# Kernel optimization log

Hardware: AMD Instinct MI355X
Metric: run time of the kernel (lower is better)

The kernel has to match this reference:

```python
import jax, jax.numpy as jnp
import numpy as np

N, E = 50000, 800000
IN_DIM, HID, OUT_DIM = 128, 96, 64
MAX_REC = 5


def setup_inputs() -> dict:
    key = jax.random.key(0)
    ks = jax.random.split(key, 10)
    g = lambda k, shape, scale: (jax.random.normal(k, shape, jnp.float32) * scale)
    return {
        "x": jax.random.normal(ks[0], (N, IN_DIM), jnp.float32),
        "edge_index": jax.random.randint(ks[1], (2, E), 0, N, jnp.int32),
        "w_in": g(ks[2], (IN_DIM, HID), 0.05),
        "b_in": jnp.zeros((HID,), jnp.float32),
        "tau_w1": g(ks[3], (IN_DIM, 16), 0.08),
        "tau_b1": jnp.zeros((16,), jnp.float32),
        "tau_w2": g(ks[4], (16, 1), 0.25),
        "tau_b2": jnp.zeros((1,), jnp.float32),
        "gru_wih": g(ks[5], (3 * HID, HID), 0.05),
        "gru_whh": g(ks[6], (3 * HID, HID), 0.05),
        "gru_bih": jnp.zeros((3 * HID,), jnp.float32),
        "gru_bhh": jnp.zeros((3 * HID,), jnp.float32),
        "w_out": g(ks[7], (HID, OUT_DIM), 0.05),
        "b_out": jnp.zeros((OUT_DIM,), jnp.float32),
    }


def _gru_cell(inp, h, wih, whh, bih, bhh):
    # torch.nn.GRUCell math; wih/whh are [3H, H] stacked (r, z, n)
    gi = inp @ wih.T + bih  # [N, 3H]
    gh = h @ whh.T + bhh    # [N, 3H]
    ir, iz, inn = jnp.split(gi, 3, axis=-1)
    hr, hz, hn = jnp.split(gh, 3, axis=-1)
    r = jax.nn.sigmoid(ir + hr)
    z = jax.nn.sigmoid(iz + hz)
    n = jnp.tanh(inn + r * hn)
    return (1.0 - z) * n + z * h


def reference(x, edge_index, w_in, b_in, tau_w1, tau_b1, tau_w2, tau_b2,
              gru_wih, gru_whh, gru_bih, gru_bhh, w_out, b_out):
    h = jax.nn.relu(x @ w_in + b_in)  # [N, H]
    tau_val = jax.nn.softplus(jax.nn.relu(x @ tau_w1 + tau_b1) @ tau_w2 + tau_b2)[:, 0]
    # .long() truncates toward zero; tau > 0 so trunc == floor via int cast
    steps = jnp.minimum((1.0 / tau_val).astype(jnp.int32), MAX_REC)  # [N]
    row, col = edge_index[0], edge_index[1]
    for _ in range(MAX_REC):
        d1 = jnp.abs(h[row] - h[col])                       # [E, H]
        agg = jax.ops.segment_sum(d1, row, num_segments=N)  # [N, H]
        new_h = _gru_cell(agg, h, gru_wih, gru_whh, gru_bih, gru_bhh)
        h = jnp.where((steps > 0)[:, None], new_h, h)
        steps = steps - 1
    return h @ w_out + b_out
```

## Files before the change

kernel.cpp:

```cpp
#include <hip/hip_runtime.h>
#include <hip/hip_bf16.h>

#define HID 96
#define INDIM 128
#define OUTDIM 64
#define BM 128
#define GP 128

typedef __attribute__((ext_vector_type(8))) _Float16 half8;
typedef __attribute__((ext_vector_type(4))) _Float16 half4;
typedef __attribute__((ext_vector_type(4))) float floatx4;

__device__ __forceinline__ float ldmix(const void* p, long i, int mode) {
    return mode ? ((const float*)p)[i]
                : __bfloat162float(((const __hip_bfloat16*)p)[i]);
}

__global__ void sniff_kernel(const unsigned int* xw, int* mode) {
    int lane = threadIdx.x & 63;
    int cnt = 0;
    for (int i = lane; i < 4096; i += 64) {
        unsigned int low = xw[i] & 0xFFFFu;
        unsigned int e = (low >> 7) & 0xFFu;
        if (e >= 0xC0u) cnt++;
    }
    #pragma unroll
    for (int ofs = 32; ofs > 0; ofs >>= 1) cnt += __shfl_down(cnt, ofs);
    if (lane == 0) *mode = (cnt > 256) ? 1 : 0;
}

__global__ void prep_kernel(const void* w_in, const void* b_in, const void* tau_w1,
                            const void* tau_b1, const void* tau_w2, const void* tau_b2,
                            const void* wih, const void* whh, const void* bih, const void* bhh,
                            const void* w_out, const void* b_out,
                            _Float16* W2F, _Float16* WinF, _Float16* WoutF,
                            float* tau_w1_f, float* smallf, const int* mode) {
    int m = *mode;
    int tid = blockIdx.x*blockDim.x + threadIdx.x;
    if (tid < 384*192) {
        int c = tid / 192, k = tid % 192;
        int g = c / 96, jj = c % 96;
        float v = 0.f;
        if (k < 96) {
            if (g == 0)      v = ldmix(wih, (long)(jj)*96 + k, m);
            else if (g == 1) v = ldmix(wih, (long)(96+jj)*96 + k, m);
            else if (g == 2) v = ldmix(wih, (long)(192+jj)*96 + k, m);
        } else {
            int kk = k - 96;
            if (g == 0)      v = ldmix(whh, (long)(jj)*96 + kk, m);
            else if (g == 1) v = ldmix(whh, (long)(96+jj)*96 + kk, m);
            else if (g == 3) v = ldmix(whh, (long)(192+jj)*96 + kk, m);
        }
        W2F[tid] = (_Float16)v;
    }
    if (tid < 96*128) {
        int j = tid >> 7, k = tid & 127;
        WinF[tid] = (_Float16)ldmix(w_in, (long)k*96 + j, m);
    }
    if (tid < 64*96) {
        int j = tid / 96, k = tid % 96;
        WoutF[tid] = (_Float16)ldmix(w_out, (long)k*OUTDIM + j, m);
    }
    if (tid < INDIM*16)   tau_w1_f[tid] = ldmix(tau_w1, tid, m);
    if (tid < HID)    smallf[tid]       = ldmix(b_in, tid, m);
    if (tid < 3*HID){ smallf[96+tid]    = ldmix(bih, tid, m);
                      smallf[384+tid]   = ldmix(bhh, tid, m); }
    if (tid < OUTDIM) smallf[672+tid]   = ldmix(b_out, tid, m);
    if (tid < 16)   { smallf[736+tid]   = ldmix(tau_w2, tid, m);
                      smallf[752+tid]   = ldmix(tau_b1, tid, m); }
    if (tid == 0)     smallf[768]       = ldmix(tau_b2, 0, m);
}

__global__ void __launch_bounds__(512) h0_kernel(
        const void* __restrict__ x, const _Float16* __restrict__ WinF,
        const float* __restrict__ smallf, const int* __restrict__ mode,
        _Float16* __restrict__ hN, int N) {
    int row0 = blockIdx.x * BM;
    int jj0 = blockIdx.y * 16;

    __shared__ _Float16 Ah[128*136];
    __shared__ _Float16 Wh[16*136];

    int tid = threadIdx.x;
    int m = *mode;
    long limit = (long)N * INDIM;
    #pragma unroll
    for (int j = 0; j < 8; j++) {
        int e = (tid + j*512) * 4;
        int r = e >> 7, c = e & 127;
        long ge = (long)(row0 + r)*INDIM + c;
        half4 vh = {0, 0, 0, 0};
        if (ge + 4 <= limit) {
            if (m) {
                floatx4 v = *(const floatx4*)((const float*)x + ge);
                #pragma unroll
                for (int q = 0; q < 4; q++) vh[q] = (_Float16)v[q];
            } else {
                const __hip_bfloat16* p = (const __hip_bfloat16*)x + ge;
                #pragma unroll
                for (int q = 0; q < 4; q++) vh[q] = (_Float16)__bfloat162float(p[q]);
            }
        }
        *(half4*)(&Ah[r*136 + c]) = vh;
    }
    if (tid < 256) {
        int wrow = tid >> 4;
        int k = (tid & 15) * 8;
        *(half8*)(&Wh[wrow*136 + k]) = *(const half8*)(WinF + (long)(jj0 + wrow)*INDIM + k);
    }
    __syncthreads();

    int lane = tid & 63;
    int w = tid >> 6;
    int m15 = lane & 15, quad = lane >> 4;
    floatx4 acc = {0.f, 0.f, 0.f, 0.f};
    int abase = (w*16 + m15)*136 + quad*8;
    #pragma unroll
    for (int ks = 0; ks < 4; ks++) {
        int k0 = ks*32;
        half8 a = *(const half8*)(&Ah[abase + k0]);
        half8 b = *(const half8*)(&Wh[m15*136 + quad*8 + k0]);
        acc = __builtin_amdgcn_mfma_f32_16x16x32_f16(a, b, acc, 0, 0, 0);
    }

    int jj = jj0 + m15;
    float b = smallf[jj];
    #pragma unroll
    for (int reg = 0; reg < 4; reg++) {
        int li = row0 + w*16 + quad*4 + reg;
        if (li < N) hN[(long)li*HID + jj] = (_Float16)fmaxf(acc[reg] + b, 0.f);
    }
}

__global__ void __launch_bounds__(128) tau_kernel(
        const void* __restrict__ x, const float* __restrict__ tau_w1_f,
        const float* __restrict__ smallf, const int* __restrict__ mode,
        int* __restrict__ steps, int N) {
    __shared__ float xs[128*129];
    __shared__ float ws[2048];
    __shared__ float wb[34];

    int tid = threadIdx.x;
    int row0 = blockIdx.x * 128;
    int m = *mode;

    #pragma unroll
    for (int j = 0; j < 16; j++) ws[tid + j*128] = tau_w1_f[tid + j*128];
    if (tid < 16) { wb[tid] = smallf[752 + tid]; wb[16 + tid] = smallf[736 + tid]; }
    if (tid == 32) wb[32] = smallf[768];

    for (int j = 0; j < 128; j++) {
        int n = row0 + j;
        float v = 0.f;
        if (n < N) {
            long ge = (long)n*INDIM + tid;
            v = m ? ((const float*)x)[ge]
                  : __bfloat162float(((const __hip_bfloat16*)x)[ge]);
        }
        xs[j*129 + tid] = v;
    }
    __syncthreads();

    int n = row0 + tid;
    float acc[16];
    #pragma unroll
    for (int j = 0; j < 16; j++) acc[j] = 0.f;
    const float* xr = &xs[tid*129];
    for (int k = 0; k < 128; k++) {
        float xv = xr[k];
        const float* w = &ws[k*16];
        #pragma unroll
        for (int j = 0; j < 16; j++) acc[j] += xv * w[j];
    }
    float z = wb[32];
    #pragma unroll
    for (int j = 0; j < 16; j++) z += fmaxf(acc[j] + wb[j], 0.f) * wb[16 + j];
    float tau = fmaxf(z, 0.f) + log1pf(expf(-fabsf(z)));
    float inv = 1.0f / tau;
    int s;
    if (inv >= 5.0f) s = 5;
    else { s = (int)inv; if (s < 0) s = 0; if (s > 5) s = 5; }
    if (n < N) steps[n] = s;
}

__global__ void partial_kernel(const int* __restrict__ steps, const int* __restrict__ deg,
                               int N, int C, int* __restrict__ blksum) {
    __shared__ int red[256*8];
    int tid = threadIdx.x;
    int tg = blockIdx.x*256 + tid;
    int start = tg*C, end = min(start + C, N);
    if (end < start) end = start;
    int cnt[7] = {0,0,0,0,0,0,0};
    for (int i = start; i < end; i++) { cnt[steps[i]]++; cnt[6] += deg[i]; }
    #pragma unroll
    for (int k = 0; k < 7; k++) red[tid*8 + k] = cnt[k];
    __syncthreads();
    for (int ofs = 128; ofs > 0; ofs >>= 1) {
        if (tid < ofs) {
            #pragma unroll
            for (int k = 0; k < 7; k++) red[tid*8 + k] += red[(tid+ofs)*8 + k];
        }
        __syncthreads();
    }
    if (tid < 7) blksum[blockIdx.x*8 + tid] = red[tid];
}

__global__ void base_kernel(const int* __restrict__ blksum, int* __restrict__ bstart,
                            int* __restrict__ blkbase, int* __restrict__ off, int N) {
    __shared__ int tot[8];
    __shared__ int sb[8];
    int tid = threadIdx.x;
    if (tid < 7) {
        int s = 0;
        for (int b = 0; b < GP; b++) s += blksum[b*8 + tid];
        tot[tid] = s;
    }
    __syncthreads();
    if (tid == 0) {
        int run = 0;
        for (int ss = 5; ss >= 0; --ss) { sb[ss] = run; bstart[ss] = run; run += tot[ss]; }
        bstart[6] = run;
        off[N] = tot[6];
        sb[6] = 0;
    }
    __syncthreads();
    if (tid < 7) {
        int run = sb[tid];
        for (int b = 0; b < GP; b++) { blkbase[b*8 + tid] = run; run += blksum[b*8 + tid]; }
    }
}

__global__ void scatter_kernel(const int* __restrict__ steps, const int* __restrict__ deg,
                               const int* __restrict__ blkbase, int N, int C,
                               int* __restrict__ order, int* __restrict__ off) {
    __shared__ int buf[256];
    int tid = threadIdx.x;
    int b = blockIdx.x;
    int tg = b*256 + tid;
    int start = tg*C, end = min(start + C, N);
    if (end < start) end = start;
    int cnt[7] = {0,0,0,0,0,0,0};
    for (int i = start; i < end; i++) { cnt[steps[i]]++; cnt[6] += deg[i]; }
    int mybase[7];
    #pragma unroll
    for (int k = 0; k < 7; k++) {
        buf[tid] = cnt[k];
        __syncthreads();
        for (int ofs = 1; ofs < 256; ofs <<= 1) {
            int t = (tid >= ofs) ? buf[tid - ofs] : 0;
            __syncthreads();
            buf[tid] += t;
            __syncthreads();
        }
        mybase[k] = blkbase[b*8 + k] + buf[tid] - cnt[k];
        __syncthreads();
    }
    for (int i = start; i < end; i++) {
        int s = steps[i];
        order[mybase[s]++] = i;
        off[i] = mybase[6];
        mybase[6] += deg[i];
    }
}

__global__ void pack_kernel(const _Float16* __restrict__ hN, const int* __restrict__ order,
                            _Float16* __restrict__ hF, int N) {
    int tid = blockIdx.x*blockDim.x + threadIdx.x;
    if (tid >= N*HID) return;
    int li = tid / HID, f = tid % HID;
    int n = order[li];
    hF[tid] = hN[(size_t)n*HID + f];
}

__global__ void deg_kernel(const int* __restrict__ row, int* deg, int E) {
    int e = blockIdx.x*blockDim.x + threadIdx.x;
    if (e < E) atomicAdd(&deg[row[e]], 1);
}

__global__ void fill_kernel(const int* __restrict__ row, const int* __restrict__ col,
                            const int* __restrict__ off, int* cur, int* __restrict__ csr_col, int E) {
    int e = blockIdx.x*blockDim.x + threadIdx.x;
    if (e >= E) return;
    int r = row[e];
    int p = atomicAdd(&cur[r], 1);
    csr_col[off[r] + p] = col[e];
}

__global__ void agg_kernel(const _Float16* __restrict__ hN, const int* __restrict__ off,
                           const int* __restrict__ csr_col, const int* __restrict__ order,
                           const int* __restrict__ bstart, int t, _Float16* __restrict__ aggF) {
    int K = bstart[t];
    int total = K * 12;
    int stride = gridDim.x * blockDim.x;
    for (int idx = blockIdx.x*blockDim.x + threadIdx.x; idx < total; idx += stride) {
        int li = idx / 12, fg = idx % 12;
        int f = fg * 8;
        int i = order[li];
        half8 hv = *(const half8*)(hN + (size_t)i*HID + f);
        float hvf[8];
        #pragma unroll
        for (int q = 0; q < 8; q++) hvf[q] = (float)hv[q];
        int e0 = off[i], e1 = off[i+1];
        float acc[8];
        #pragma unroll
        for (int q = 0; q < 8; q++) acc[q] = 0.f;
        int e = e0;
        for (; e + 4 <= e1; e += 4) {
            int c0 = csr_col[e],   c1 = csr_col[e+1];
            int c2 = csr_col[e+2], c3 = csr_col[e+3];
            half8 v0 = *(const half8*)(hN + (size_t)c0*HID + f);
            half8 v1 = *(const half8*)(hN + (size_t)c1*HID + f);
            half8 v2 = *(const half8*)(hN + (size_t)c2*HID + f);
            half8 v3 = *(const half8*)(hN + (size_t)c3*HID + f);
            #pragma unroll
            for (int q = 0; q < 8; q++) {
                acc[q] += fabsf(hvf[q] - (float)v0[q]) + fabsf(hvf[q] - (float)v1[q])
                        + fabsf(hvf[q] - (float)v2[q]) + fabsf(hvf[q] - (float)v3[q]);
            }
        }
        for (; e < e1; e++) {
            int c = csr_col[e];
            half8 v = *(const half8*)(hN + (size_t)c*HID + f);
            #pragma unroll
            for (int q = 0; q < 8; q++) acc[q] += fabsf(hvf[q] - (float)v[q]);
        }
        half8 outv;
        #pragma unroll
        for (int q = 0; q < 8; q++) outv[q] = (_Float16)acc[q];
        *(half8*)(aggF + (size_t)li*HID + f) = outv;
    }
}

__global__ void __launch_bounds__(512) gru_kernel(
        const _Float16* __restrict__ aggF, const _Float16* __restrict__ hFin,
        const _Float16* __restrict__ W2F,
        const float* __restrict__ smallf, const int* __restrict__ bstart, int t,
        const int* __restrict__ order, _Float16* __restrict__ hN,
        _Float16* __restrict__ hFout, int N) {
    int K = bstart[t];
    int row0 = blockIdx.x * BM;
    if (row0 >= K) return;
    int jj0 = blockIdx.y * 16;

    __shared__ _Float16 Ah[128*200];
    __shared__ _Float16 Wh[64*200];

    int tid = threadIdx.x;
    long limit = (long)N * HID;
    #pragma unroll
    for (int j = 0; j < 3; j++) {
        int e = (tid + j*512) * 8;
        {
            int r = e / 96, c = e % 96;
            long ge = (long)(row0 + r)*96 + c;
            half8 va = {0,0,0,0,0,0,0,0}, vh = va;
            if (ge + 8 <= limit) {
                va = *(const half8*)(aggF + ge);
                vh = *(const half8*)(hFin + ge);
            }
            *(half8*)(&Ah[r*200 + c])      = va;
            *(half8*)(&Ah[r*200 + 96 + c]) = vh;
        }
        {
            int wrow = e / 192, k = e % 192;
            int g = wrow >> 4, cc = wrow & 15;
            *(half8*)(&Wh[wrow*200 + k]) = *(const half8*)(W2F + (long)(g*96 + jj0 + cc)*192 + k);
        }
    }
    __syncthreads();

    int lane = tid & 63;
    int w = tid >> 6;
    int m15 = lane & 15, quad = lane >> 4;
    floatx4 acc[4];
    #pragma unroll
    for (int g = 0; g < 4; g++) acc[g] = (floatx4){0.f, 0.f, 0.f, 0.f};

    int abase = (w*16 + m15)*200 + quad*8;
    #pragma unroll
    for (int ks = 0; ks < 6; ks++) {
        int k0 = ks*32;
        half8 a = *(const half8*)(&Ah[abase + k0]);
        #pragma unroll
        for (int g = 0; g < 4; g++) {
            half8 b = *(const half8*)(&Wh[(g*16 + m15)*200 + quad*8 + k0]);
            acc[g] = __builtin_amdgcn_mfma_f32_16x16x32_f16(a, b, acc[g], 0, 0, 0);
        }
    }

    int jj = jj0 + m15;
    float bir = smallf[96+jj],  biz = smallf[192+jj], bin = smallf[288+jj];
    float bhr = smallf[384+jj], bhz = smallf[480+jj], bhn = smallf[576+jj];
    #pragma unroll
    for (int reg = 0; reg < 4; reg++) {
        int li = row0 + w*16 + quad*4 + reg;
        if (li < K) {
            float rp = acc[0][reg] + bir + bhr;
            float zp = acc[1][reg] + biz + bhz;
            float ip = acc[2][reg] + bin;
            float hn = acc[3][reg] + bhn;
            float r  = 1.f/(1.f + expf(-rp));
            float z  = 1.f/(1.f + expf(-zp));
            float nn = tanhf(ip + r*hn);
            int tr = w*16 + quad*4 + reg;
            float hold = (float)Ah[tr*200 + 96 + jj];
            _Float16 v16 = (_Float16)((1.f - z)*nn + z*hold);
            int node = order[li];
            hN[(long)node*HID + jj] = v16;
            hFout[(long)li*HID + jj] = v16;
        }
    }
}

__global__ void __launch_bounds__(512) out_kernel(
        const _Float16* __restrict__ hN, const _Float16* __restrict__ WoutF,
        const float* __restrict__ smallf, void* out, const int* mode, int N) {
    int row0 = blockIdx.x * BM;
    int jj0 = blockIdx.y * 16;

    __shared__ _Float16 Ah[128*104];
    __shared__ _Float16 Wh[16*104];

    int tid = threadIdx.x;
    long limit = (long)N * HID;
    #pragma unroll
    for (int j = 0; j < 3; j++) {
        int e = (tid + j*512) * 8;
        int r = e / 96, c = e % 96;
        long ge = (long)(row0 + r)*HID + c;
        half8 v = {0,0,0,0,0,0,0,0};
        if (ge + 8 <= limit) v = *(const half8*)(hN + ge);
        *(half8*)(&Ah[r*104 + c]) = v;
    }
    if (tid < 192) {
        int wrow = tid / 12;
        int k = (tid % 12) * 8;
        *(half8*)(&Wh[wrow*104 + k]) = *(const half8*)(WoutF + (long)(jj0 + wrow)*HID + k);
    }
    __syncthreads();

    int lane = tid & 63;
    int w = tid >> 6;
    int m15 = lane & 15, quad = lane >> 4;
    floatx4 acc = {0.f, 0.f, 0.f, 0.f};
    int abase = (w*16 + m15)*104 + quad*8;
    #pragma unroll
    for (int ks = 0; ks < 3; ks++) {
        int k0 = ks*32;
        half8 a = *(const half8*)(&Ah[abase + k0]);
        half8 b = *(const half8*)(&Wh[m15*104 + quad*8 + k0]);
        acc = __builtin_amdgcn_mfma_f32_16x16x32_f16(a, b, acc, 0, 0, 0);
    }

    int jj = jj0 + m15;
    float b = smallf[672+jj];
    int m = *mode;
    #pragma unroll
    for (int reg = 0; reg < 4; reg++) {
        int li = row0 + w*16 + quad*4 + reg;
        if (li < N) {
            float v = acc[reg] + b;
            long oi = (long)li*OUTDIM + jj;
            if (m) ((float*)out)[oi] = v;
            else   ((__hip_bfloat16*)out)[oi] = __float2bfloat16(v);
        }
    }
}

extern "C" void kernel_launch(void* const* d_in, const int* in_sizes, int n_in,
                              void* d_out, int out_size, void* d_ws, size_t ws_size,
                              hipStream_t stream) {
    const void* x      = d_in[0];
    const int*  ei     = (const int*)d_in[1];
    const void* w_in   = d_in[2],  *b_in   = d_in[3];
    const void* tau_w1 = d_in[4],  *tau_b1 = d_in[5];
    const void* tau_w2 = d_in[6],  *tau_b2 = d_in[7];
    const void* wih    = d_in[8],  *whh    = d_in[9];
    const void* bih    = d_in[10], *bhh    = d_in[11];
    const void* w_out  = d_in[12], *b_out  = d_in[13];

    int N = in_sizes[0] / INDIM;
    int E = in_sizes[1] / 2;
    const int* row = ei;
    const int* col = ei + E;

    char* ws = (char*)d_ws;
    size_t o = 0;
    auto take = [&](size_t bytes) -> char* {
        char* p = ws + o;
        o = (o + bytes + 255) & ~(size_t)255;
        return p;
    };
    _Float16* hN    = (_Float16*)take((size_t)N*HID*2);
    _Float16* hFa   = (_Float16*)take((size_t)N*HID*2);
    _Float16* hFb   = (_Float16*)take((size_t)N*HID*2);
    _Float16* aggF  = (_Float16*)take((size_t)N*HID*2);
    _Float16* W2F   = (_Float16*)take((size_t)384*192*2);
    _Float16* WinF  = (_Float16*)take((size_t)96*128*2);
    _Float16* WoutF = (_Float16*)take((size_t)64*96*2);
    float* tau_w1_f = (float*)take((size_t)INDIM*16*4);
    float* smallf   = (float*)take(1024*4);
    int*   off      = (int*)take((size_t)(N+1)*4);
    int*   csr_col  = (int*)take((size_t)E*4);
    int*   order    = (int*)take((size_t)N*4);
    int*   steps    = (int*)take((size_t)N*4);
    int*   bstart   = (int*)take(64);
    int*   mode     = (int*)take(64);
    int*   blksum   = (int*)take((size_t)GP*8*4);
    int*   blkbase  = (int*)take((size_t)GP*8*4);
    char*  zbase    = ws + o;
    int*   deg      = (int*)take((size_t)N*4);
    int*   cur      = (int*)take((size_t)N*4);
    size_t zbytes   = (size_t)((ws + o) - zbase);

    hipMemsetAsync(zbase, 0, zbytes, stream);
    sniff_kernel<<<1, 64, 0, stream>>>((const unsigned int*)x, mode);

    prep_kernel<<<(384*192 + 255)/256, 256, 0, stream>>>(
        w_in, b_in, tau_w1, tau_b1, tau_w2, tau_b2, wih, whh, bih, bhh, w_out, b_out,
        W2F, WinF, WoutF, tau_w1_f, smallf, mode);

    dim3 hgrid((N + BM - 1)/BM, 6);
    h0_kernel<<<hgrid, 512, 0, stream>>>(x, WinF, smallf, mode, hN, N);
    tau_kernel<<<(N + 127)/128, 128, 0, stream>>>(x, tau_w1_f, smallf, mode, steps, N);
    deg_kernel<<<(E + 255)/256, 256, 0, stream>>>(row, deg, E);

    int C = (N + GP*256 - 1) / (GP*256);
    partial_kernel<<<GP, 256, 0, stream>>>(steps, deg, N, C, blksum);
    base_kernel<<<1, 64, 0, stream>>>(blksum, bstart, blkbase, off, N);
    scatter_kernel<<<GP, 256, 0, stream>>>(steps, deg, blkbase, N, C, order, off);

    pack_kernel<<<(N*HID + 255)/256, 256, 0, stream>>>(hN, order, hFa, N);
    fill_kernel<<<(E + 255)/256, 256, 0, stream>>>(row, col, off, cur, csr_col, E);

    dim3 ggrid((N + BM - 1)/BM, 6);
    _Float16* hin = hFa;
    _Float16* hout = hFb;
    for (int t = 0; t < 5; t++) {
        agg_kernel<<<4096, 256, 0, stream>>>(hN, off, csr_col, order, bstart, t, aggF);
        gru_kernel<<<ggrid, 512, 0, stream>>>(aggF, hin, W2F, smallf, bstart, t,
                                              order, hN, hout, N);
        _Float16* tmp = hin; hin = hout; hout = tmp;
    }

    dim3 ogrid((N + BM - 1)/BM, 4);
    out_kernel<<<ogrid, 512, 0, stream>>>(hN, WoutF, smallf, d_out, mode, N);
}
```

Before: 421.9 us.

## Build CSR via two-level binned counting sort instead of global atomics

```diff
diff --git a/kernel.cpp b/kernel.cpp
--- a/kernel.cpp
+++ b/kernel.cpp
@@ -6,6 +6,7 @@
 #define OUTDIM 64
 #define BM 128
 #define GP 128
+#define NBMAX 2048
 
 typedef __attribute__((ext_vector_type(8))) _Float16 half8;
 typedef __attribute__((ext_vector_type(4))) _Float16 half4;
@@ -183,34 +184,146 @@
     if (n < N) steps[n] = s;
 }
 
-__global__ void partial_kernel(const int* __restrict__ steps, const int* __restrict__ deg,
-                               int N, int C, int* __restrict__ blksum) {
+__global__ void bincnt_kernel(const int* __restrict__ row, int E, int NB, int shift,
+                              int* __restrict__ bincnt) {
+    __shared__ int h[NBMAX];
+    int tid = threadIdx.x;
+    for (int i = tid; i < NB; i += 256) h[i] = 0;
+    __syncthreads();
+    int stride = gridDim.x * blockDim.x;
+    for (int e = blockIdx.x*blockDim.x + tid; e < E; e += stride)
+        atomicAdd(&h[row[e] >> shift], 1);
+    __syncthreads();
+    for (int i = tid; i < NB; i += 256) {
+        int c = h[i];
+        if (c) atomicAdd(&bincnt[i], c);
+    }
+}
+
+__global__ void binscan_kernel(const int* __restrict__ bincnt, int NB, int E, int N,
+                               int* __restrict__ bin_start, int* __restrict__ bincur,
+                               int* __restrict__ off) {
+    __shared__ int vals[NBMAX];
+    __shared__ int part[256];
+    int tid = threadIdx.x;
+    int per = (NB + 255) / 256;
+    int base = tid * per;
+    int s = 0;
+    for (int j = 0; j < per; j++) {
+        int i = base + j;
+        int v = (i < NB) ? bincnt[i] : 0;
+        if (i < NBMAX) vals[i] = s;
+        s += v;
+    }
+    part[tid] = s;
+    __syncthreads();
+    for (int ofs = 1; ofs < 256; ofs <<= 1) {
+        int t = (tid >= ofs) ? part[tid - ofs] : 0;
+        __syncthreads();
+        part[tid] += t;
+        __syncthreads();
+    }
+    int add = (tid == 0) ? 0 : part[tid - 1];
+    for (int j = 0; j < per; j++) {
+        int i = base + j;
+        if (i < NB) {
+            int v = vals[i] + add;
+            bin_start[i] = v;
+            bincur[i] = v;
+        }
+    }
+    if (tid == 0) { bin_start[NB] = E; off[N] = E; }
+}
+
+__global__ void binfill_kernel(const int* __restrict__ row, const int* __restrict__ col,
+                               int E, int NB, int shift, int* __restrict__ bincur,
+                               unsigned int* __restrict__ binbuf) {
+    __shared__ int h[NBMAX];
+    __shared__ int bs[NBMAX];
+    int tid = threadIdx.x;
+    int chunk = (E + gridDim.x - 1) / gridDim.x;
+    int c0 = blockIdx.x * chunk;
+    int c1 = min(c0 + chunk, E);
+    for (int i = tid; i < NB; i += 256) h[i] = 0;
+    __syncthreads();
+    for (int e = c0 + tid; e < c1; e += 256)
+        atomicAdd(&h[row[e] >> shift], 1);
+    __syncthreads();
+    for (int i = tid; i < NB; i += 256) {
+        int c = h[i];
+        if (c) { bs[i] = atomicAdd(&bincur[i], c); h[i] = 0; }
+    }
+    __syncthreads();
+    int mask = (1 << shift) - 1;
+    for (int e = c0 + tid; e < c1; e += 256) {
+        int r = row[e];
+        int b = r >> shift;
+        int p = atomicAdd(&h[b], 1);
+        binbuf[bs[b] + p] = ((unsigned int)(r & mask) << 24) | (unsigned int)col[e];
+    }
+}
+
+__global__ void bincsr_kernel(const unsigned int* __restrict__ binbuf,
+                              const int* __restrict__ bin_start, int N, int shift,
+                              int* __restrict__ off, int* __restrict__ csr_col) {
+    __shared__ int hist[256];
+    __shared__ int pfx[256];
+    int b = blockIdx.x;
+    int tid = threadIdx.x;
+    int BINSZ = 1 << shift;
+    int s0 = bin_start[b], s1 = bin_start[b + 1];
+    for (int i = tid; i < BINSZ; i += 128) hist[i] = 0;
+    __syncthreads();
+    for (int e = s0 + tid; e < s1; e += 128)
+        atomicAdd(&hist[binbuf[e] >> 24], 1);
+    __syncthreads();
+    if (tid == 0) {
+        int run = 0;
+        for (int j = 0; j < BINSZ; j++) { pfx[j] = run; run += hist[j]; }
+    }
+    __syncthreads();
+    if (tid < BINSZ) {
+        int node = (b << shift) + tid;
+        if (node < N) off[node] = s0 + pfx[tid];
+        hist[tid] = pfx[tid];
+    }
+    __syncthreads();
+    for (int e = s0 + tid; e < s1; e += 128) {
+        unsigned int pk = binbuf[e];
+        int lr = pk >> 24;
+        int p = atomicAdd(&hist[lr], 1);
+        csr_col[s0 + p] = (int)(pk & 0xFFFFFFu);
+    }
+}
+
+__global__ void partial_kernel(const int* __restrict__ steps, int N, int C,
+                               int* __restrict__ blksum) {
     __shared__ int red[256*8];
     int tid = threadIdx.x;
     int tg = blockIdx.x*256 + tid;
     int start = tg*C, end = min(start + C, N);
     if (end < start) end = start;
-    int cnt[7] = {0,0,0,0,0,0,0};
-    for (int i = start; i < end; i++) { cnt[steps[i]]++; cnt[6] += deg[i]; }
-    #pragma unroll
-    for (int k = 0; k < 7; k++) red[tid*8 + k] = cnt[k];
+    int cnt[6] = {0,0,0,0,0,0};
+    for (int i = start; i < end; i++) cnt[steps[i]]++;
+    #pragma unroll
+    for (int k = 0; k < 6; k++) red[tid*8 + k] = cnt[k];
     __syncthreads();
     for (int ofs = 128; ofs > 0; ofs >>= 1) {
         if (tid < ofs) {
             #pragma unroll
-            for (int k = 0; k < 7; k++) red[tid*8 + k] += red[(tid+ofs)*8 + k];
+            for (int k = 0; k < 6; k++) red[tid*8 + k] += red[(tid+ofs)*8 + k];
         }
         __syncthreads();
     }
-    if (tid < 7) blksum[blockIdx.x*8 + tid] = red[tid];
+    if (tid < 6) blksum[blockIdx.x*8 + tid] = red[tid];
 }
 
 __global__ void base_kernel(const int* __restrict__ blksum, int* __restrict__ bstart,
-                            int* __restrict__ blkbase, int* __restrict__ off, int N) {
+                            int* __restrict__ blkbase) {
     __shared__ int tot[8];
     __shared__ int sb[8];
     int tid = threadIdx.x;
-    if (tid < 7) {
+    if (tid < 6) {
         int s = 0;
         for (int b = 0; b < GP; b++) s += blksum[b*8 + tid];
         tot[tid] = s;
@@ -220,30 +333,27 @@
         int run = 0;
         for (int ss = 5; ss >= 0; --ss) { sb[ss] = run; bstart[ss] = run; run += tot[ss]; }
         bstart[6] = run;
-        off[N] = tot[6];
-        sb[6] = 0;
-    }
-    __syncthreads();
-    if (tid < 7) {
+    }
+    __syncthreads();
+    if (tid < 6) {
         int run = sb[tid];
         for (int b = 0; b < GP; b++) { blkbase[b*8 + tid] = run; run += blksum[b*8 + tid]; }
     }
 }
 
-__global__ void scatter_kernel(const int* __restrict__ steps, const int* __restrict__ deg,
-                               const int* __restrict__ blkbase, int N, int C,
-                               int* __restrict__ order, int* __restrict__ off) {
+__global__ void scatter_kernel(const int* __restrict__ steps, const int* __restrict__ blkbase,
+                               int N, int C, int* __restrict__ order) {
     __shared__ int buf[256];
     int tid = threadIdx.x;
     int b = blockIdx.x;
     int tg = b*256 + tid;
     int start = tg*C, end = min(start + C, N);
     if (end < start) end = start;
-    int cnt[7] = {0,0,0,0,0,0,0};
-    for (int i = start; i < end; i++) { cnt[steps[i]]++; cnt[6] += deg[i]; }
-    int mybase[7];
-    #pragma unroll
-    for (int k = 0; k < 7; k++) {
+    int cnt[6] = {0,0,0,0,0,0};
+    for (int i = start; i < end; i++) cnt[steps[i]]++;
+    int mybase[6];
+    #pragma unroll
+    for (int k = 0; k < 6; k++) {
         buf[tid] = cnt[k];
         __syncthreads();
         for (int ofs = 1; ofs < 256; ofs <<= 1) {
@@ -255,12 +365,7 @@
         mybase[k] = blkbase[b*8 + k] + buf[tid] - cnt[k];
         __syncthreads();
     }
-    for (int i = start; i < end; i++) {
-        int s = steps[i];
-        order[mybase[s]++] = i;
-        off[i] = mybase[6];
-        mybase[6] += deg[i];
-    }
+    for (int i = start; i < end; i++) order[mybase[steps[i]]++] = i;
 }
 
 __global__ void pack_kernel(const _Float16* __restrict__ hN, const int* __restrict__ order,
@@ -270,20 +375,6 @@
     int li = tid / HID, f = tid % HID;
     int n = order[li];
     hF[tid] = hN[(size_t)n*HID + f];
-}
-
-__global__ void deg_kernel(const int* __restrict__ row, int* deg, int E) {
-    int e = blockIdx.x*blockDim.x + threadIdx.x;
-    if (e < E) atomicAdd(&deg[row[e]], 1);
-}
-
-__global__ void fill_kernel(const int* __restrict__ row, const int* __restrict__ col,
-                            const int* __restrict__ off, int* cur, int* __restrict__ csr_col, int E) {
-    int e = blockIdx.x*blockDim.x + threadIdx.x;
-    if (e >= E) return;
-    int r = row[e];
-    int p = atomicAdd(&cur[r], 1);
-    csr_col[off[r] + p] = col[e];
 }
 
 __global__ void agg_kernel(const _Float16* __restrict__ hN, const int* __restrict__ off,
@@ -484,6 +575,10 @@
     const int* row = ei;
     const int* col = ei + E;
 
+    int shift = 5;
+    while ((((N + (1 << shift) - 1) >> shift)) > NBMAX && shift < 8) shift++;
+    int NB = (N + (1 << shift) - 1) >> shift;
+
     char* ws = (char*)d_ws;
     size_t o = 0;
     auto take = [&](size_t bytes) -> char* {
@@ -508,9 +603,11 @@
     int*   mode     = (int*)take(64);
     int*   blksum   = (int*)take((size_t)GP*8*4);
     int*   blkbase  = (int*)take((size_t)GP*8*4);
+    unsigned int* binbuf = (unsigned int*)take((size_t)E*4);
+    int*   bin_start = (int*)take((size_t)(NBMAX+1)*4);
+    int*   bincur    = (int*)take((size_t)NBMAX*4);
     char*  zbase    = ws + o;
-    int*   deg      = (int*)take((size_t)N*4);
-    int*   cur      = (int*)take((size_t)N*4);
+    int*   bincnt   = (int*)take((size_t)NBMAX*4);
     size_t zbytes   = (size_t)((ws + o) - zbase);
 
     hipMemsetAsync(zbase, 0, zbytes, stream);
@@ -523,15 +620,18 @@
     dim3 hgrid((N + BM - 1)/BM, 6);
     h0_kernel<<<hgrid, 512, 0, stream>>>(x, WinF, smallf, mode, hN, N);
     tau_kernel<<<(N + 127)/128, 128, 0, stream>>>(x, tau_w1_f, smallf, mode, steps, N);
-    deg_kernel<<<(E + 255)/256, 256, 0, stream>>>(row, deg, E);
+
+    bincnt_kernel<<<64, 256, 0, stream>>>(row, E, NB, shift, bincnt);
+    binscan_kernel<<<1, 256, 0, stream>>>(bincnt, NB, E, N, bin_start, bincur, off);
+    binfill_kernel<<<64, 256, 0, stream>>>(row, col, E, NB, shift, bincur, binbuf);
+    bincsr_kernel<<<NB, 128, 0, stream>>>(binbuf, bin_start, N, shift, off, csr_col);
 
     int C = (N + GP*256 - 1) / (GP*256);
-    partial_kernel<<<GP, 256, 0, stream>>>(steps, deg, N, C, blksum);
-    base_kernel<<<1, 64, 0, stream>>>(blksum, bstart, blkbase, off, N);
-    scatter_kernel<<<GP, 256, 0, stream>>>(steps, deg, blkbase, N, C, order, off);
+    partial_kernel<<<GP, 256, 0, stream>>>(steps, N, C, blksum);
+    base_kernel<<<1, 64, 0, stream>>>(blksum, bstart, blkbase);
+    scatter_kernel<<<GP, 256, 0, stream>>>(steps, blkbase, N, C, order);
 
     pack_kernel<<<(N*HID + 255)/256, 256, 0, stream>>>(hN, order, hFa, N);
-    fill_kernel<<<(E + 255)/256, 256, 0, stream>>>(row, col, off, cur, csr_col, E);
 
     dim3 ggrid((N + BM - 1)/BM, 6);
     _Float16* hin = hFa;
```

New measurement: 406.8 us. 3.6% less time.
